# Performance work log

Hardware: AMD Instinct MI355X
Metric: run time of the kernel (lower is better)

## Reference

```python
import jax, jax.numpy as jnp
import numpy as np

D = 768       # input_size
C = 8000      # num_classes
S = 4096      # seq_len
B = 2         # batch
SCALE = 1.0
LN_EPS = 1e-5


def setup_inputs() -> dict:
    key = jax.random.key(0)
    ks = jax.random.split(key, 8)
    std = 0.03  # module's _init_weights std
    return {
        "x": jax.random.normal(ks[0], (B, S, D), dtype=jnp.float32),
        "encoded_descriptions": jax.random.normal(ks[1], (C, D), dtype=jnp.float32),
        "Wk": jax.random.normal(ks[2], (D, D), dtype=jnp.float32) * std,
        "Wv": jax.random.normal(ks[3], (D, D), dtype=jnp.float32) * std,
        "bv": jax.random.normal(ks[4], (D,), dtype=jnp.float32) * 0.01,
        "ln_gamma": jnp.ones((D,), dtype=jnp.float32),
        "ln_beta": jnp.zeros((D,), dtype=jnp.float32),
        "out_w": jax.random.normal(ks[5], (D,), dtype=jnp.float32) * std,
        "out_b": jax.random.normal(ks[6], (), dtype=jnp.float32) * 0.01,
    }


def reference(x, encoded_descriptions, Wk, Wv, bv, ln_gamma, ln_beta, out_w, out_b):
    # V = x @ Wv^T + bv ; K = x @ Wk^T  (torch Linear applies weight transposed)
    V = jnp.einsum('bsd,ed->bse', x, Wv) + bv          # [B, S, D]
    K = jnp.einsum('bsd,ed->bse', x, Wk)               # [B, S, D]
    # att_weights = Q @ K^T, Q broadcast over batch -> [B, C, S]
    att = jnp.einsum('cd,bsd->bcs', encoded_descriptions, K)
    attention = jax.nn.softmax(att / SCALE, axis=2)    # [B, C, S]
    y = jnp.einsum('bcs,bsd->bcd', attention, V)       # [B, C, D]
    # LayerNorm over last dim
    mu = jnp.mean(y, axis=-1, keepdims=True)
    var = jnp.mean(jnp.square(y - mu), axis=-1, keepdims=True)
    y = (y - mu) * jax.lax.rsqrt(var + LN_EPS) * ln_gamma + ln_beta
    # output = sum over D of out_w * y + out_b  -> [B, C]
    out = jnp.einsum('bcd,d->bc', y, out_w) + out_b
    return out
```

## Files before the change

kernel.cpp:

```cpp
#include <hip/hip_runtime.h>


typedef _Float16 half8  __attribute__((ext_vector_type(8)));
typedef _Float16 half4v __attribute__((ext_vector_type(4)));
typedef float    f32x4  __attribute__((ext_vector_type(4)));
typedef float    f32x16 __attribute__((ext_vector_type(16)));

#define L2E 1.44269504088896340736f

__device__ __forceinline__ void gld_lds16(_Float16* lds, const _Float16* g) {
  __builtin_amdgcn_global_load_lds(
      (const __attribute__((address_space(1))) unsigned int*)g,
      (__attribute__((address_space(3))) unsigned int*)lds, 16, 0, 0);
}

__global__ void cvt_kernel(const float* __restrict__ src, _Float16* __restrict__ dst, int n4) {
  int i = blockIdx.x * blockDim.x + threadIdx.x;
  if (i >= n4) return;
  float4 v = reinterpret_cast<const float4*>(src)[i];
  half4v h; h[0] = (_Float16)v.x; h[1] = (_Float16)v.y; h[2] = (_Float16)v.z; h[3] = (_Float16)v.w;
  reinterpret_cast<half4v*>(dst)[i] = h;
}

template <int MODE>
__global__ __launch_bounds__(256, 2) void gemm_nt_f16(
    const _Float16* __restrict__ A, const _Float16* __restrict__ Bt,
    _Float16* __restrict__ C, const float* __restrict__ bias, int M, int N)
{
  __shared__ __align__(16) _Float16 As[2][128 * 64];
  __shared__ __align__(16) _Float16 Bs[2][128 * 64];
  const int tid = threadIdx.x;
  const int lane = tid & 63, wid = tid >> 6;
  const int ntn = N >> 7;
  const int mtile = blockIdx.x / ntn, ntile = blockIdx.x - mtile * ntn;
  const int m0 = mtile << 7, n0 = ntile << 7;
  const int wm = wid >> 1, wn = wid & 1;

  f32x4 acc[4][4] = {};

  auto stage = [&](int buf, int kt) {
#pragma unroll
    for (int j = 0; j < 4; ++j) {
      int idx = (j << 8) + tid;
      int row = idx >> 3, slot = idx & 7;
      int gc = (kt << 6) + ((slot ^ (row & 7)) << 3);
      _Float16* ldsbase_a = &As[buf][(size_t)(((j << 8) + (wid << 6)) << 3)];
      _Float16* ldsbase_b = &Bs[buf][(size_t)(((j << 8) + (wid << 6)) << 3)];
      gld_lds16(ldsbase_a, &A[(size_t)(m0 + row) * 768 + gc]);
      gld_lds16(ldsbase_b, &Bt[(size_t)(n0 + row) * 768 + gc]);
    }
  };

  stage(0, 0);
  __syncthreads();

  for (int kt = 0; kt < 12; ++kt) {
    int cur = kt & 1;
    if (kt < 11) stage(cur ^ 1, kt + 1);
#pragma unroll
    for (int ks = 0; ks < 2; ++ks) {
      half8 a[4], b[4];
      int dloc = (ks << 5) + ((lane >> 4) << 3);
#pragma unroll
      for (int mi = 0; mi < 4; ++mi) {
        int row = (wm << 6) + (mi << 4) + (lane & 15);
        a[mi] = *reinterpret_cast<const half8*>(&As[cur][row * 64 + (dloc ^ ((row & 7) << 3))]);
      }
#pragma unroll
      for (int ni = 0; ni < 4; ++ni) {
        int row = (wn << 6) + (ni << 4) + (lane & 15);
        b[ni] = *reinterpret_cast<const half8*>(&Bs[cur][row * 64 + (dloc ^ ((row & 7) << 3))]);
      }
#pragma unroll
      for (int mi = 0; mi < 4; ++mi)
#pragma unroll
        for (int ni = 0; ni < 4; ++ni)
          acc[mi][ni] = __builtin_amdgcn_mfma_f32_16x16x32_f16(a[mi], b[ni], acc[mi][ni], 0, 0, 0);
    }
    __syncthreads();
  }

#pragma unroll
  for (int mi = 0; mi < 4; ++mi)
#pragma unroll
    for (int ni = 0; ni < 4; ++ni) {
      int col = n0 + (wn << 6) + (ni << 4) + (lane & 15);
#pragma unroll
      for (int r = 0; r < 4; ++r) {
        int row = m0 + (wm << 6) + (mi << 4) + ((lane >> 4) << 2) + r;
        float v = acc[mi][ni][r];
        if (bias) v += bias[row];
        size_t a;
        if (MODE == 1) {
          a = ((size_t)(row >> 5) * 48 + (col >> 4)) * 512 + (row & 31) * 16 + (col & 15);
        } else {
          a = (((size_t)(col >> 12) * 24 + (row >> 5)) * 256 + ((col & 4095) >> 4)) * 512
              + (row & 31) * 16 + (col & 15);
        }
        C[a] = (_Float16)v;
      }
    }
}

#define QS_STRIDE 776
#define PS_STRIDE 264

__global__ __launch_bounds__(512, 2) void attn_kernel(
    const float* __restrict__ Qf, const _Float16* __restrict__ Kf,
    const _Float16* __restrict__ Vf,
    const float* __restrict__ gamma, const float* __restrict__ beta,
    const float* __restrict__ outw, const float* __restrict__ outb,
    float* __restrict__ out)
{
  __shared__ __align__(16) _Float16 Qs[64 * QS_STRIDE];
  __shared__ __align__(16) _Float16 Ps[64 * PS_STRIDE];
  __shared__ float redmax[8 * 64];
  __shared__ float redsum[8 * 64];
  __shared__ float gws[768];
  __shared__ float epi[64 * 25];
  __shared__ float lrowS[64];
  __shared__ float scal[2];

  const int tid = threadIdx.x;
  const int lane = tid & 63;
  const int wid = tid >> 6;
  const int l31 = lane & 31;
  const int lh = lane >> 5;

  int xcd = blockIdx.x & 7, i8 = blockIdx.x >> 3;
  int f = (xcd < 2) ? (xcd * 32 + i8) : (64 + (xcd - 2) * 31 + i8);
  const int bb = f / 125;
  const int ct = f - bb * 125;
  const int c0 = ct << 6;

#pragma unroll
  for (int i = 0; i < 24; ++i) {
    int idx = tid + (i << 9);
    int row = idx / 192, c4 = idx - row * 192;
    float4 v = reinterpret_cast<const float4*>(Qf)[(size_t)(c0 + row) * 192 + c4];
    half4v h; h[0] = (_Float16)v.x; h[1] = (_Float16)v.y; h[2] = (_Float16)v.z; h[3] = (_Float16)v.w;
    *reinterpret_cast<half4v*>(&Qs[row * QS_STRIDE + (c4 << 2)]) = h;
  }
  for (int i = tid; i < 768; i += 512) gws[i] = gamma[i] * outw[i];
  __syncthreads();
  if (tid < 64) {
    float g = 0.f, bw = 0.f;
#pragma unroll
    for (int j = 0; j < 12; ++j) { int d = tid + (j << 6); g += gws[d]; bw += beta[d] * outw[d]; }
#pragma unroll
    for (int m = 32; m; m >>= 1) { g += __shfl_xor(g, m); bw += __shfl_xor(bw, m); }
    if (tid == 0) { scal[0] = g; scal[1] = bw; }
  }

  float mrow0 = -1e30f, mrow1 = -1e30f, lrow0 = 0.f, lrow1 = 0.f;

  f32x16 acc00 = {}, acc01 = {}, acc02 = {};
  f32x16 acc10 = {}, acc11 = {}, acc12 = {};
  const int n0w = wid * 96;
  const _Float16* qrow0 = &Qs[l31 * QS_STRIDE + (lh << 3)];
  const _Float16* qrow1 = qrow0 + 32 * QS_STRIDE;
  const int laneoff = l31 * 16 + lh * 8;
  const _Float16* kfb = Kf + ((size_t)(bb * 128 + wid) * 48) * 512 + laneoff;
  const _Float16* vfb = Vf + ((size_t)(bb * 24 + wid * 3) * 256) * 512 + laneoff;

  for (int st = 0; st < 16; ++st) {
    f32x16 qk0 = {}, qk1 = {};
    const _Float16* kb = kfb + (size_t)st * (8 * 48 * 512);
    uint4 kp[4];
#pragma unroll
    for (int j = 0; j < 4; ++j) kp[j] = *reinterpret_cast<const uint4*>(kb + j * 512);
#pragma unroll
    for (int k = 0; k < 48; ++k) {
      half8 kf = __builtin_bit_cast(half8, kp[k & 3]);
      if (k < 44) kp[k & 3] = *reinterpret_cast<const uint4*>(kb + (k + 4) * 512);
      half8 qf0 = *reinterpret_cast<const half8*>(qrow0 + (k << 4));
      half8 qf1 = *reinterpret_cast<const half8*>(qrow1 + (k << 4));
      qk0 = __builtin_amdgcn_mfma_f32_32x32x16_f16(kf, qf0, qk0, 0, 0, 0);
      qk1 = __builtin_amdgcn_mfma_f32_32x32x16_f16(kf, qf1, qk1, 0, 0, 0);
    }
    const _Float16* vb = vfb + (size_t)st * (16 * 512);
    uint4 vp[2][3];
    vp[0][0] = *reinterpret_cast<const uint4*>(vb);
    vp[0][1] = *reinterpret_cast<const uint4*>(vb + 131072);
    vp[0][2] = *reinterpret_cast<const uint4*>(vb + 262144);

    float mx0 = qk0[0], mx1 = qk1[0];
#pragma unroll
    for (int r = 1; r < 16; ++r) { mx0 = fmaxf(mx0, qk0[r]); mx1 = fmaxf(mx1, qk1[r]); }
    mx0 = fmaxf(mx0, __shfl_xor(mx0, 32));
    mx1 = fmaxf(mx1, __shfl_xor(mx1, 32));
    if (lh == 0) {
      redmax[(wid << 6) + l31] = mx0;
      redmax[(wid << 6) + 32 + l31] = mx1;
    }
    __syncthreads();
    float pm0 = redmax[l31], pm1 = redmax[32 + l31];
#pragma unroll
    for (int w = 1; w < 8; ++w) {
      pm0 = fmaxf(pm0, redmax[(w << 6) + l31]);
      pm1 = fmaxf(pm1, redmax[(w << 6) + 32 + l31]);
    }
    float mn0 = fmaxf(mrow0, pm0), mn1 = fmaxf(mrow1, pm1);
    float rr0 = exp2f((mrow0 - mn0) * L2E), rr1 = exp2f((mrow1 - mn1) * L2E);
    mrow0 = mn0; mrow1 = mn1;

    float sum0 = 0.f, sum1 = 0.f;
    const int sb = (wid << 5) + (lh << 2);
#pragma unroll
    for (int q2 = 0; q2 < 4; ++q2) {
      float p0 = exp2f((qk0[4 * q2 + 0] - mn0) * L2E);
      float p1 = exp2f((qk0[4 * q2 + 1] - mn0) * L2E);
      float p2 = exp2f((qk0[4 * q2 + 2] - mn0) * L2E);
      float p3 = exp2f((qk0[4 * q2 + 3] - mn0) * L2E);
      sum0 += (p0 + p1) + (p2 + p3);
      half4v h; h[0] = (_Float16)p0; h[1] = (_Float16)p1; h[2] = (_Float16)p2; h[3] = (_Float16)p3;
      *reinterpret_cast<half4v*>(&Ps[l31 * PS_STRIDE + sb + (q2 << 3)]) = h;
      float u0 = exp2f((qk1[4 * q2 + 0] - mn1) * L2E);
      float u1 = exp2f((qk1[4 * q2 + 1] - mn1) * L2E);
      float u2 = exp2f((qk1[4 * q2 + 2] - mn1) * L2E);
      float u3 = exp2f((qk1[4 * q2 + 3] - mn1) * L2E);
      sum1 += (u0 + u1) + (u2 + u3);
      half4v h2; h2[0] = (_Float16)u0; h2[1] = (_Float16)u1; h2[2] = (_Float16)u2; h2[3] = (_Float16)u3;
      *reinterpret_cast<half4v*>(&Ps[(32 + l31) * PS_STRIDE + sb + (q2 << 3)]) = h2;
    }
    sum0 += __shfl_xor(sum0, 32);
    sum1 += __shfl_xor(sum1, 32);
    if (lh == 0) {
      redsum[(wid << 6) + l31] = sum0;
      redsum[(wid << 6) + 32 + l31] = sum1;
    }
#pragma unroll
    for (int r = 0; r < 16; ++r) {
      int crow = (r & 3) + ((r >> 2) << 3) + (lh << 2);
      float rs0 = __shfl(rr0, crow);
      float rs1 = __shfl(rr1, crow);
      acc00[r] *= rs0; acc01[r] *= rs0; acc02[r] *= rs0;
      acc10[r] *= rs1; acc11[r] *= rs1; acc12[r] *= rs1;
    }
    vp[1][0] = *reinterpret_cast<const uint4*>(vb + 512);
    vp[1][1] = *reinterpret_cast<const uint4*>(vb + 131072 + 512);
    vp[1][2] = *reinterpret_cast<const uint4*>(vb + 262144 + 512);
    __syncthreads();
    {
      float s0 = redsum[l31], s1 = redsum[32 + l31];
#pragma unroll
      for (int w = 1; w < 8; ++w) {
        s0 += redsum[(w << 6) + l31];
        s1 += redsum[(w << 6) + 32 + l31];
      }
      lrow0 = lrow0 * rr0 + s0;
      lrow1 = lrow1 * rr1 + s1;
    }
#pragma unroll
    for (int ks = 0; ks < 16; ++ks) {
      half8 b0 = __builtin_bit_cast(half8, vp[ks & 1][0]);
      half8 b1 = __builtin_bit_cast(half8, vp[ks & 1][1]);
      half8 b2 = __builtin_bit_cast(half8, vp[ks & 1][2]);
      if (ks < 14) {
        vp[ks & 1][0] = *reinterpret_cast<const uint4*>(vb + (ks + 2) * 512);
        vp[ks & 1][1] = *reinterpret_cast<const uint4*>(vb + 131072 + (ks + 2) * 512);
        vp[ks & 1][2] = *reinterpret_cast<const uint4*>(vb + 262144 + (ks + 2) * 512);
      }
      half8 pa0 = *reinterpret_cast<const half8*>(&Ps[l31 * PS_STRIDE + (ks << 4) + (lh << 3)]);
      half8 pa1 = *reinterpret_cast<const half8*>(&Ps[(32 + l31) * PS_STRIDE + (ks << 4) + (lh << 3)]);
      acc00 = __builtin_amdgcn_mfma_f32_32x32x16_f16(pa0, b0, acc00, 0, 0, 0);
      acc01 = __builtin_amdgcn_mfma_f32_32x32x16_f16(pa0, b1, acc01, 0, 0, 0);
      acc02 = __builtin_amdgcn_mfma_f32_32x32x16_f16(pa0, b2, acc02, 0, 0, 0);
      acc10 = __builtin_amdgcn_mfma_f32_32x32x16_f16(pa1, b0, acc10, 0, 0, 0);
      acc11 = __builtin_amdgcn_mfma_f32_32x32x16_f16(pa1, b1, acc11, 0, 0, 0);
      acc12 = __builtin_amdgcn_mfma_f32_32x32x16_f16(pa1, b2, acc12, 0, 0, 0);
    }
  }

  if (wid == 0 && lh == 0) { lrowS[l31] = lrow0; lrowS[32 + l31] = lrow1; }
  float gw0 = gws[n0w + l31];
  float gw1 = gws[n0w + 32 + l31];
  float gw2 = gws[n0w + 64 + l31];
#pragma unroll
  for (int r = 0; r < 16; ++r) {
    int c = (r & 3) + ((r >> 2) << 3) + (lh << 2);
    {
      float y0 = acc00[r], y1 = acc01[r], y2 = acc02[r];
      float t1 = y0 + y1 + y2;
      float t2 = y0 * y0 + y1 * y1 + y2 * y2;
      float t3 = y0 * gw0 + y1 * gw1 + y2 * gw2;
#pragma unroll
      for (int m = 1; m <= 16; m <<= 1) {
        t1 += __shfl_xor(t1, m); t2 += __shfl_xor(t2, m); t3 += __shfl_xor(t3, m);
      }
      if (l31 == 0) { float* e = &epi[c * 25 + wid * 3]; e[0] = t1; e[1] = t2; e[2] = t3; }
    }
    {
      float y0 = acc10[r], y1 = acc11[r], y2 = acc12[r];
      float t1 = y0 + y1 + y2;
      float t2 = y0 * y0 + y1 * y1 + y2 * y2;
      float t3 = y0 * gw0 + y1 * gw1 + y2 * gw2;
#pragma unroll
      for (int m = 1; m <= 16; m <<= 1) {
        t1 += __shfl_xor(t1, m); t2 += __shfl_xor(t2, m); t3 += __shfl_xor(t3, m);
      }
      if (l31 == 0) { float* e = &epi[(32 + c) * 25 + wid * 3]; e[0] = t1; e[1] = t2; e[2] = t3; }
    }
  }
  __syncthreads();
  if (tid < 64) {
    float S1 = 0.f, S2 = 0.f, S3 = 0.f;
#pragma unroll
    for (int w = 0; w < 8; ++w) {
      const float* e = &epi[tid * 25 + w * 3];
      S1 += e[0]; S2 += e[1]; S3 += e[2];
    }
    float l = lrowS[tid];
    float invl = 1.0f / l;
    float mu = S1 * invl * (1.0f / 768.0f);
    float ey2 = S2 * invl * invl * (1.0f / 768.0f);
    float var = ey2 - mu * mu;
    float rs = rsqrtf(var + 1e-5f);
    float res = rs * (S3 * invl - mu * scal[0]) + scal[1] + outb[0];
    out[bb * 8000 + c0 + tid] = res;
  }
}

extern "C" void kernel_launch(void* const* d_in, const int* in_sizes, int n_in,
                              void* d_out, int out_size, void* d_ws, size_t ws_size,
                              hipStream_t stream) {
  (void)in_sizes; (void)n_in; (void)out_size; (void)ws_size;
  const float* x     = (const float*)d_in[0];
  const float* qenc  = (const float*)d_in[1];
  const float* Wk    = (const float*)d_in[2];
  const float* Wv    = (const float*)d_in[3];
  const float* bv    = (const float*)d_in[4];
  const float* gam   = (const float*)d_in[5];
  const float* bet   = (const float*)d_in[6];
  const float* outw  = (const float*)d_in[7];
  const float* outb  = (const float*)d_in[8];
  float* out = (float*)d_out;

  char* ws = (char*)d_ws;
  _Float16* x_h  = (_Float16*)(ws);
  _Float16* wk_h = (_Float16*)(ws + 12582912);
  _Float16* wv_h = (_Float16*)(ws + 13762560);
  _Float16* K_f  = (_Float16*)(ws + 14942208);
  _Float16* V_f  = (_Float16*)(ws + 27525120);

  cvt_kernel<<<6144, 256, 0, stream>>>(x, x_h, 1572864);
  cvt_kernel<<<576, 256, 0, stream>>>(Wk, wk_h, 147456);
  cvt_kernel<<<576, 256, 0, stream>>>(Wv, wv_h, 147456);
  gemm_nt_f16<1><<<384, 256, 0, stream>>>(x_h, wk_h, K_f, nullptr, 8192, 768);
  gemm_nt_f16<2><<<384, 256, 0, stream>>>(wv_h, x_h, V_f, bv, 768, 8192);
  attn_kernel<<<250, 512, 0, stream>>>(qenc, K_f, V_f, gam, bet, outw, outb, out);
}
```

Baseline: 318.1 us.

## Prefetch next-tile K/V across iterations and skip rescale when max is unchanged

```diff
diff --git a/kernel.cpp b/kernel.cpp
--- a/kernel.cpp
+++ b/kernel.cpp
@@ -12,6 +12,11 @@
   __builtin_amdgcn_global_load_lds(
       (const __attribute__((address_space(1))) unsigned int*)g,
       (__attribute__((address_space(3))) unsigned int*)lds, 16, 0, 0);
+}
+__device__ __forceinline__ void gld_touch4(_Float16* lds, const _Float16* g) {
+  __builtin_amdgcn_global_load_lds(
+      (const __attribute__((address_space(1))) unsigned int*)g,
+      (__attribute__((address_space(3))) unsigned int*)lds, 4, 0, 0);
 }
 
 __global__ void cvt_kernel(const float* __restrict__ src, _Float16* __restrict__ dst, int n4) {
@@ -114,6 +119,7 @@
 {
   __shared__ __align__(16) _Float16 Qs[64 * QS_STRIDE];
   __shared__ __align__(16) _Float16 Ps[64 * PS_STRIDE];
+  __shared__ __align__(16) _Float16 tdump[8 * 128];
   __shared__ float redmax[8 * 64];
   __shared__ float redsum[8 * 64];
   __shared__ float gws[768];
@@ -133,6 +139,23 @@
   const int ct = f - bb * 125;
   const int c0 = ct << 6;
 
+  const int n0w = wid * 96;
+  const int laneoff = l31 * 16 + lh * 8;
+  _Float16* tbase = &tdump[wid << 7];
+  const _Float16* kfb = Kf + ((size_t)(bb * 128 + wid) * 48) * 512 + laneoff;
+  const _Float16* vfb = Vf + ((size_t)(bb * 24 + wid * 3) * 256) * 512 + laneoff;
+
+  uint4 kp[4];
+#pragma unroll
+  for (int j = 0; j < 4; ++j) kp[j] = *reinterpret_cast<const uint4*>(kfb + j * 512);
+  uint4 vp[2][3];
+#pragma unroll
+  for (int j = 0; j < 2; ++j) {
+    vp[j][0] = *reinterpret_cast<const uint4*>(vfb + j * 512);
+    vp[j][1] = *reinterpret_cast<const uint4*>(vfb + 131072 + j * 512);
+    vp[j][2] = *reinterpret_cast<const uint4*>(vfb + 262144 + j * 512);
+  }
+
 #pragma unroll
   for (int i = 0; i < 24; ++i) {
     int idx = tid + (i << 9);
@@ -156,33 +179,29 @@
 
   f32x16 acc00 = {}, acc01 = {}, acc02 = {};
   f32x16 acc10 = {}, acc11 = {}, acc12 = {};
-  const int n0w = wid * 96;
   const _Float16* qrow0 = &Qs[l31 * QS_STRIDE + (lh << 3)];
   const _Float16* qrow1 = qrow0 + 32 * QS_STRIDE;
-  const int laneoff = l31 * 16 + lh * 8;
-  const _Float16* kfb = Kf + ((size_t)(bb * 128 + wid) * 48) * 512 + laneoff;
-  const _Float16* vfb = Vf + ((size_t)(bb * 24 + wid * 3) * 256) * 512 + laneoff;
-
+
+#pragma unroll 1
   for (int st = 0; st < 16; ++st) {
+    const _Float16* kb  = kfb + (size_t)st * 196608;
+    const _Float16* kbn = kb + 196608;
+    const _Float16* vb  = vfb + (size_t)st * 8192;
+    const _Float16* vbn = vb + 8192;
+    const bool more = (st < 15);
+
     f32x16 qk0 = {}, qk1 = {};
-    const _Float16* kb = kfb + (size_t)st * (8 * 48 * 512);
-    uint4 kp[4];
-#pragma unroll
-    for (int j = 0; j < 4; ++j) kp[j] = *reinterpret_cast<const uint4*>(kb + j * 512);
 #pragma unroll
     for (int k = 0; k < 48; ++k) {
       half8 kf = __builtin_bit_cast(half8, kp[k & 3]);
-      if (k < 44) kp[k & 3] = *reinterpret_cast<const uint4*>(kb + (k + 4) * 512);
+      if (k < 44)      kp[k & 3] = *reinterpret_cast<const uint4*>(kb + (k + 4) * 512);
+      else if (more)   kp[k & 3] = *reinterpret_cast<const uint4*>(kbn + (k - 44) * 512);
+      if (more) gld_touch4(tbase, vbn + (k >> 4) * 131072 + (k & 15) * 512);
       half8 qf0 = *reinterpret_cast<const half8*>(qrow0 + (k << 4));
       half8 qf1 = *reinterpret_cast<const half8*>(qrow1 + (k << 4));
       qk0 = __builtin_amdgcn_mfma_f32_32x32x16_f16(kf, qf0, qk0, 0, 0, 0);
       qk1 = __builtin_amdgcn_mfma_f32_32x32x16_f16(kf, qf1, qk1, 0, 0, 0);
     }
-    const _Float16* vb = vfb + (size_t)st * (16 * 512);
-    uint4 vp[2][3];
-    vp[0][0] = *reinterpret_cast<const uint4*>(vb);
-    vp[0][1] = *reinterpret_cast<const uint4*>(vb + 131072);
-    vp[0][2] = *reinterpret_cast<const uint4*>(vb + 262144);
 
     float mx0 = qk0[0], mx1 = qk1[0];
 #pragma unroll
@@ -229,17 +248,16 @@
       redsum[(wid << 6) + l31] = sum0;
       redsum[(wid << 6) + 32 + l31] = sum1;
     }
-#pragma unroll
-    for (int r = 0; r < 16; ++r) {
-      int crow = (r & 3) + ((r >> 2) << 3) + (lh << 2);
-      float rs0 = __shfl(rr0, crow);
-      float rs1 = __shfl(rr1, crow);
-      acc00[r] *= rs0; acc01[r] *= rs0; acc02[r] *= rs0;
-      acc10[r] *= rs1; acc11[r] *= rs1; acc12[r] *= rs1;
-    }
-    vp[1][0] = *reinterpret_cast<const uint4*>(vb + 512);
-    vp[1][1] = *reinterpret_cast<const uint4*>(vb + 131072 + 512);
-    vp[1][2] = *reinterpret_cast<const uint4*>(vb + 262144 + 512);
+    if (__any(rr0 < 1.0f) || __any(rr1 < 1.0f)) {
+#pragma unroll
+      for (int r = 0; r < 16; ++r) {
+        int crow = (r & 3) + ((r >> 2) << 3) + (lh << 2);
+        float rs0 = __shfl(rr0, crow);
+        float rs1 = __shfl(rr1, crow);
+        acc00[r] *= rs0; acc01[r] *= rs0; acc02[r] *= rs0;
+        acc10[r] *= rs1; acc11[r] *= rs1; acc12[r] *= rs1;
+      }
+    }
     __syncthreads();
     {
       float s0 = redsum[l31], s1 = redsum[32 + l31];
@@ -260,6 +278,15 @@
         vp[ks & 1][0] = *reinterpret_cast<const uint4*>(vb + (ks + 2) * 512);
         vp[ks & 1][1] = *reinterpret_cast<const uint4*>(vb + 131072 + (ks + 2) * 512);
         vp[ks & 1][2] = *reinterpret_cast<const uint4*>(vb + 262144 + (ks + 2) * 512);
+      } else if (more) {
+        vp[ks & 1][0] = *reinterpret_cast<const uint4*>(vbn + (ks - 14) * 512);
+        vp[ks & 1][1] = *reinterpret_cast<const uint4*>(vbn + 131072 + (ks - 14) * 512);
+        vp[ks & 1][2] = *reinterpret_cast<const uint4*>(vbn + 262144 + (ks - 14) * 512);
+      }
+      if (more) {
+        gld_touch4(tbase, kbn + (ks * 3 + 0) * 512);
+        gld_touch4(tbase, kbn + (ks * 3 + 1) * 512);
+        gld_touch4(tbase, kbn + (ks * 3 + 2) * 512);
       }
       half8 pa0 = *reinterpret_cast<const half8*>(&Ps[l31 * PS_STRIDE + (ks << 4) + (lh << 3)]);
       half8 pa1 = *reinterpret_cast<const half8*>(&Ps[(32 + l31) * PS_STRIDE + (ks << 4) + (lh << 3)]);
```

New measurement: 516.0 us. +62.2%, slower.
